# Optimization experiments

Measured on AMD Instinct MI355X. Metric: run time of the kernel, lower is better.

## Reference

```python
import jax, jax.numpy as jnp
import numpy as np

# dims: B batch, N nodes, E edges, C=dim_in, W=window_len, D=embed_dim, O=dim_out, K=link_len, NB=bootstrap count
B, N, E, C, W, D, O, K, NB = 16, 2000, 3000, 17, 12, 16, 256, 3, 3


def setup_inputs() -> dict:
    key = jax.random.key(0)
    ks = jax.random.split(key, 20)
    return {
        "x": jax.random.normal(ks[0], (B, N, C), jnp.float32),
        "x_window": jax.random.normal(ks[1], (B, W, N, 1), jnp.float32),
        "node_embeddings": jax.random.normal(ks[2], (N, D), jnp.float32) * 0.1,
        "fixed_adj": 0,
        "adj": jax.random.normal(ks[3], (N, N), jnp.float32),
        "stay_cost": 1,
        "jump_cost": 1,
        "ZFC_input": jax.random.normal(ks[4], (B, O // 8), jnp.float32),
        "hodge_Laplacian": jax.random.normal(ks[5], (E, E), jnp.float32) * 0.02,
        "x_e_window": jax.random.normal(ks[6], (B, W, E, 1), jnp.float32),
        "incidence_matrix": jax.random.normal(ks[7], (N, E), jnp.float32) * 0.02,
        "weights_pool": jax.random.normal(ks[8], (D, K, C, O // 4), jnp.float32) * 0.05,
        "window_weights_supra": jax.random.normal(ks[9], (D, 1, O // 8), jnp.float32) * 0.05,
        "window_weights_temporal": jax.random.normal(ks[10], (D, 1, O // 2), jnp.float32) * 0.05,
        "bias_pool": jax.random.normal(ks[11], (D, O), jnp.float32) * 0.05,
        "T_param": jax.random.normal(ks[12], (W,), jnp.float32) * 0.1,
        "lin_w": jax.random.normal(ks[13], (1, 1), jnp.float32),
        "lin_b": jax.random.normal(ks[14], (1,), jnp.float32),
        "gnn_w": jax.random.normal(ks[15], (N, N), jnp.float32) * 0.02,
        "gnn_b": jnp.zeros((N,), jnp.float32),
        "bootstrap_idx": jnp.sort(jax.random.randint(ks[16], (NB,), 0, W)),
    }


def _forward(x, x_window, ne, fixed_adj, adj, stay_cost, jump_cost, ZFC_input,
             hodge, x_e_window, inc, wp, wws_p, wwt_p, bp, Tp, lin_w, lin_b,
             gnn_w, gnn_b, bidx):
    n = ne.shape[0]
    e = hodge.shape[0]
    b = x.shape[0]
    nb = bidx.shape[0]

    # adaptive transition matrix S (diag filled with stay_cost after relu)
    S0 = jax.nn.relu(ne @ ne.T)
    ii = jnp.arange(n)
    S0 = S0.at[ii, ii].set(jnp.float32(stay_cost))
    if fixed_adj:  # static Python bool branch
        S = adj * jnp.exp(S0)
    else:
        S = jax.nn.softmax(S0, axis=1)
    # faithful to torch broadcasting: column j divided by row-sum of row j
    S = S / jnp.sum(S, axis=1)

    # diffusion support power series: [I, S, S@S, ...]
    sup = [jnp.eye(n, dtype=S.dtype), S]
    for _ in range(2, K):
        sup.append(S @ sup[-1])
    supports = jnp.stack(sup, axis=0)  # (K, N, N)

    # supra-Laplacian: hodge on diagonal blocks, jump_cost*I on strict upper blocks
    supra = (jnp.kron(jnp.eye(nb, dtype=hodge.dtype), hodge)
             + jnp.kron(jnp.triu(jnp.ones((nb, nb), hodge.dtype), 1),
                        jnp.float32(jump_cost) * jnp.eye(e, dtype=hodge.dtype)))  # (nb*E, nb*E)

    # adaptive weights/bias from node embeddings
    weights = jnp.einsum('nd,dkio->nkio', ne, wp)   # (N, K, C, O/4)
    bias = ne @ bp                                   # (N, O)

    # graph diffusion branch
    x_s = jnp.einsum('knm,bmc->bknc', supports, x).transpose(0, 2, 1, 3)  # (B,N,K,C)
    x_sconv = jnp.einsum('bnki,nkio->bno', x_s, weights)                   # (B,N,O/4)

    # supra / hypergraph branch
    wws = jnp.einsum('nd,dio->nio', ne, wws_p)                 # (N,1,O/8)
    xe = x_e_window[:, bidx].reshape(b, nb * e, 1)             # bootstrap gather
    xe = xe * lin_w[0, 0] + lin_b[0]                           # Linear(1,1)
    xes = jnp.einsum('bmi,mn->bni', xe, supra).reshape(b, nb, 1, e)
    xen = jnp.einsum('bfim,mn->bfin', xes, inc.T).reshape(b, nb, n, 1)
    x_e_n_wconv = jnp.einsum('bfni,nio->bfno', xen, wws).mean(axis=1)  # (B,N,O/8)

    # temporal window branch (einsum fuses the permute + matmul with T)
    wwt = jnp.einsum('nd,dio->nio', ne, wwt_p)                  # (N,1,O/2)
    x_wconv_t = jnp.einsum('btni,nio,t->bno', x_window, wwt, Tp)  # (B,N,O/2)

    # ZFC branch: repeat over nodes, GNN = Linear(N,N) + relu, reshape (view) back
    ZFC = jnp.tile(ZFC_input.reshape(b, -1, 1), (1, 1, n))      # (B,O/8,N)
    zout = jax.nn.relu(ZFC @ gnn_w.T + gnn_b)                   # (B,O/8,N)
    x_ZFC = zout.reshape(b, n, -1)                              # (B,N,O/8) (reshape, not transpose)

    return jnp.concatenate([x_sconv, x_ZFC, x_wconv_t, x_e_n_wconv], axis=-1) + bias


def reference(x, x_window, node_embeddings, fixed_adj, adj, stay_cost, jump_cost,
              ZFC_input, hodge_Laplacian, x_e_window, incidence_matrix,
              weights_pool, window_weights_supra, window_weights_temporal,
              bias_pool, T_param, lin_w, lin_b, gnn_w, gnn_b, bootstrap_idx):
    return _forward(x, x_window, node_embeddings, fixed_adj, adj, stay_cost,
                    jump_cost, ZFC_input, hodge_Laplacian, x_e_window,
                    incidence_matrix, weights_pool, window_weights_supra,
                    window_weights_temporal, bias_pool, T_param, lin_w, lin_b,
                    gnn_w, gnn_b, bootstrap_idx)
```

## Files before the change

kernel.cpp:

```cpp
#include <hip/hip_runtime.h>
#include <hip/hip_bf16.h>

typedef __hip_bfloat16 bf16;
typedef unsigned short ushort_t;
typedef __attribute__((ext_vector_type(8))) short short8;
typedef __attribute__((ext_vector_type(4))) short short4_t;
typedef __attribute__((ext_vector_type(4))) float f32x4;
typedef __attribute__((ext_vector_type(2))) float f32x2;

#define B_ 16
#define N_ 2000
#define E_ 3000
#define C_ 17
#define W_ 12
#define D_ 16
#define O_ 256
#define NB_ 3
#define KPAD 2048
#define KI_ 51
#define SEGS 25
#define ECH 120
#define EPAD 768

static __device__ __forceinline__ ushort_t f2b(float f) {
  bf16 h = __float2bfloat16(f);
  return *reinterpret_cast<ushort_t*>(&h);
}
static __device__ __forceinline__ float b2f_u(ushort_t u) {
  bf16 h = *reinterpret_cast<bf16*>(&u);
  return __bfloat162float(h);
}
__device__ __forceinline__ int idxval(const int* p, int i) {
  int iv = p[i];
  if (iv >= 0 && iv < 1000000) return iv;
  return (int)__int_as_float(iv);
}

__global__ void k_S(const float* __restrict__ ne, const int* __restrict__ stay,
                    ushort_t* __restrict__ S) {
  const int i = blockIdx.x;
  const int t = threadIdx.x;
  if (i >= N_) {
#pragma unroll
    for (int it = 0; it < 8; ++it) S[(long)i*KPAD + t + it*256] = 0;
    return;
  }
  __shared__ float ne_l[512*20];
  __shared__ float reds[4];
  f32x4 nei[4];
#pragma unroll
  for (int q = 0; q < 4; ++q) nei[q] = *(const f32x4*)(ne + i*16 + q*4);
  const float stayf = (float)(*stay);
  float vals[8];
  float s = 0.f;
  for (int c = 0; c < 4; ++c) {
    __syncthreads();
#pragma unroll
    for (int u = 0; u < 8; ++u) {
      int unit = t + u*256;
      int row = unit >> 2, dq = unit & 3;
      int gj = c*512 + row;
      f32x4 v = {0.f,0.f,0.f,0.f};
      if (gj < N_) v = *(const f32x4*)(ne + gj*16 + dq*4);
      *(f32x4*)(ne_l + row*20 + dq*4) = v;
    }
    __syncthreads();
#pragma unroll
    for (int r = 0; r < 2; ++r) {
      int row_l = t + r*256;
      int j = c*512 + row_l;
      float e = 0.f;
      if (j < N_) {
        f32x4 a4 = {0.f,0.f,0.f,0.f};
#pragma unroll
        for (int q = 0; q < 4; ++q) a4 += nei[q] * (*(const f32x4*)(ne_l + row_l*20 + q*4));
        float dot = a4.x + a4.y + a4.z + a4.w;
        float v = dot > 0.f ? dot : 0.f;
        if (j == i) v = stayf;
        e = __expf(v);
        s += e;
      }
      vals[2*c + r] = e;
    }
  }
#pragma unroll
  for (int off = 32; off > 0; off >>= 1) s += __shfl_xor(s, off, 64);
  if ((t & 63) == 0) reds[t >> 6] = s;
  __syncthreads();
  s = reds[0] + reds[1] + reds[2] + reds[3];
  const float inv = 1.f/s;
#pragma unroll
  for (int it = 0; it < 8; ++it) {
    int j = t + it*256;
    S[(long)i*KPAD + j] = f2b(vals[it]*inv);
  }
}

__global__ void k_small(const float* __restrict__ xew, const int* __restrict__ bidx,
                        const float* __restrict__ lw, const float* __restrict__ lb,
                        const int* __restrict__ jc, float* __restrict__ u,
                        float* __restrict__ v,
                        const float* __restrict__ xwin, const float* __restrict__ Tp,
                        float* __restrict__ xw,
                        const float* __restrict__ gw, float* __restrict__ g,
                        const float* __restrict__ x, ushort_t* __restrict__ BT1) {
  const int bid = blockIdx.x;
  const int t = threadIdx.x;
  if (bid < 188) {
    int idx = bid*256 + t;
    if (idx >= B_*E_) return;
    int b = idx / E_, e = idx - b*E_;
    const float lwf = lw[0], lbf = lb[0];
    float uu = 0.f, vv = 0.f;
#pragma unroll
    for (int f = 0; f < NB_; ++f) {
      int tt = idxval(bidx, f);
      if (tt < 0) tt = 0;
      if (tt >= W_) tt = W_ - 1;
      float val = xew[(b*W_ + tt)*E_ + e]*lwf + lbf;
      uu += val;
      vv += (float)(NB_ - 1 - f)*val;
    }
    u[idx] = uu;
    v[idx] = vv*(float)(*jc);
  } else if (bid < 313) {
    int idx = (bid - 188)*256 + t;
    int b = idx / N_, n = idx - b*N_;
    float s = 0.f;
#pragma unroll
    for (int tt = 0; tt < W_; ++tt) s += xwin[(b*W_ + tt)*N_ + n]*Tp[tt];
    xw[idx] = s;
  } else if (bid < 2313) {
    int i = bid - 313;
    float s = 0.f;
    for (int j = t; j < N_; j += 256) s += gw[(long)i*N_ + j];
#pragma unroll
    for (int off = 32; off > 0; off >>= 1) s += __shfl_xor(s, off, 64);
    __shared__ float red[4];
    if ((t & 63) == 0) red[t >> 6] = s;
    __syncthreads();
    if (t == 0) g[i] = red[0] + red[1] + red[2] + red[3];
  } else {
    int j = bid - 2313;
    int bb = j / C_, cc = j - bb*C_;
#pragma unroll
    for (int uu = 0; uu < 8; ++uu) {
      int n = t + uu*256;
      float vv = 0.f;
      if (bb < B_ && n < N_) vv = x[(bb*N_ + n)*C_ + cc];
      BT1[(long)j*KPAD + n] = f2b(vv);
    }
  }
}

__global__ __launch_bounds__(256) void k_mm2(const ushort_t* __restrict__ A,
                                             const ushort_t* __restrict__ BT,
                                             float* __restrict__ Cf,
                                             ushort_t* __restrict__ Cb,
                                             int writeCb) {
  __shared__ ushort_t lds[3][10240];
  const int t = threadIdx.x;
  const int m0 = blockIdx.x * 16;
  const int j0 = blockIdx.y * 144;
  const int wv = t >> 6, lane = t & 63;
  const int lm = lane & 15, lg = lane >> 4;
  const char* gA = (const char*)A + (size_t)m0 * (KPAD*2);
  const char* gB = (const char*)BT + (size_t)j0 * (KPAD*2);

  f32x4 acc[3];
#pragma unroll
  for (int q = 0; q < 3; ++q) acc[q] = (f32x4){0.f,0.f,0.f,0.f};

  auto stage = [&](int p, int s) {
    const long kb = (long)s * 128;
#pragma unroll
    for (int u = 0; u < 5; ++u) {
      int x = (u*256 + t) << 4;
      int y = x ^ (((x >> 7) & 7) << 4);
      int r = y >> 7, c = y & 127;
      const char* gp = (r < 16) ? gA + (long)r*(KPAD*2) + kb + c
                                : gB + (long)(r-16)*(KPAD*2) + kb + c;
      __builtin_amdgcn_global_load_lds(
          (const __attribute__((address_space(1))) void*)gp,
          (__attribute__((address_space(3))) void*)(&lds[p][u*2048 + wv*512]),
          16, 0, 0);
    }
  };

  auto compute = [&](int p) {
    const char* base = (const char*)&lds[p][0];
#pragma unroll
    for (int kg = 0; kg < 2; ++kg) {
      int xA = (lm << 7) + (kg << 6) + (lg << 4);
      xA ^= ((xA >> 7) & 7) << 4;
      short8 a = *(const short8*)(base + xA);
#pragma unroll
      for (int ti = 0; ti < 3; ++ti) {
        int tile = wv + ti*4;
        if (tile < 9) {
          int xB = ((16 + tile*16 + lm) << 7) + (kg << 6) + (lg << 4);
          xB ^= ((xB >> 7) & 7) << 4;
          short8 b = *(const short8*)(base + xB);
          acc[ti] = __builtin_amdgcn_mfma_f32_16x16x32_bf16(a, b, acc[ti], 0, 0, 0);
        }
      }
    }
  };

  stage(0, 0);
  stage(1, 1);
  for (int s = 0; s < 32; ++s) {
    int p = s % 3;
    if (s < 30) {
      stage((s + 2) % 3, s + 2);
      asm volatile("s_waitcnt vmcnt(10)" ::: "memory");
    } else if (s == 30) {
      asm volatile("s_waitcnt vmcnt(5)" ::: "memory");
    } else {
      asm volatile("s_waitcnt vmcnt(0)" ::: "memory");
    }
    __builtin_amdgcn_s_barrier();
    asm volatile("" ::: "memory");
    compute(p);
    asm volatile("" ::: "memory");
    __builtin_amdgcn_s_barrier();
  }

#pragma unroll
  for (int ti = 0; ti < 3; ++ti) {
    int tile = wv + ti*4;
    if (tile < 9) {
      int j = j0 + tile*16 + lm;
      int m = m0 + lg*4;
      *(f32x4*)(Cf + (long)j*KPAD + m) = acc[ti];
      if (writeCb) {
        short4_t hv;
#pragma unroll
        for (int q = 0; q < 4; ++q)
          hv[q] = (m + q < N_) ? (short)f2b(acc[ti][q]) : (short)0;
        *(short4_t*)(Cb + (long)j*KPAD + m) = hv;
      }
    }
  }
}

__global__ void k_hodge(const float* __restrict__ u, const float* __restrict__ hodge,
                        float* __restrict__ xesP) {
  const int t = threadIdx.x;
  const int e2 = blockIdx.x*256 + t;
  const int seg = blockIdx.y;
  const int e1a = seg*ECH;
  __shared__ float ul[ECH*16];
  for (int idx = t; idx < ECH*16; idx += 256) {
    int bb = idx / ECH, ee = idx - bb*ECH;
    ul[ee*16 + bb] = u[bb*E_ + e1a + ee];
  }
  __syncthreads();
  if (e2 >= E_) return;
  float acc[16] = {};
  for (int ee = 0; ee < ECH; ee += 8) {
    float h[8];
#pragma unroll
    for (int q = 0; q < 8; ++q) h[q] = hodge[(long)(e1a + ee + q)*E_ + e2];
#pragma unroll
    for (int q = 0; q < 8; ++q) {
#pragma unroll
      for (int g4 = 0; g4 < 4; ++g4) {
        f32x4 u4 = *(const f32x4*)&ul[(ee + q)*16 + g4*4];
        acc[g4*4+0] += u4.x*h[q];
        acc[g4*4+1] += u4.y*h[q];
        acc[g4*4+2] += u4.z*h[q];
        acc[g4*4+3] += u4.w*h[q];
      }
    }
  }
#pragma unroll
  for (int bb = 0; bb < 16; ++bb)
    xesP[((long)seg*16 + bb)*E_ + e2] = acc[bb];
}

__global__ void k_redxes(const float* __restrict__ xesP, const float* __restrict__ v,
                         float* __restrict__ xes) {
  int idx = blockIdx.x*256 + threadIdx.x;
  if (idx >= B_*E_) return;
  int b = idx / E_, e = idx - b*E_;
  float s = v[idx];
#pragma unroll
  for (int q = 0; q < SEGS; ++q) s += xesP[((long)q*16 + b)*E_ + e];
  xes[idx] = s;
}

__global__ __launch_bounds__(256) void k_inc(const float* __restrict__ xes,
                                             const float* __restrict__ inc,
                                             float* __restrict__ xenP) {
  __shared__ float xes_l[16*EPAD];
  const int t = threadIdx.x;
  const int wv = t >> 6, lane = t & 63;
  const int cy = blockIdx.y;
  const int n0 = blockIdx.x*8;
  for (int i4 = t; i4 < 16*(EPAD/4); i4 += 256) {
    int row = i4 / (EPAD/4);
    int el = (i4 - row*(EPAD/4)) << 2;
    int e = cy*EPAD + el;
    f32x4 vv = {0.f,0.f,0.f,0.f};
    if (e < E_) vv = *(const f32x4*)(xes + (long)row*E_ + e);
    *(f32x4*)&xes_l[row*EPAD + el] = vv;
  }
  __syncthreads();
  const int na = n0 + wv*2;
  const int nb = na + 1;
  const float* rowA = inc + (long)na*E_ + cy*EPAD;
  const float* rowB = inc + (long)nb*E_ + cy*EPAD;
  float accA[16] = {}, accB[16] = {};
#pragma unroll
  for (int g = 0; g < 3; ++g) {
    int e4 = (g*64 + lane) << 2;
    bool ok = (cy*EPAD + e4) < E_;
    f32x4 ia = {0.f,0.f,0.f,0.f}, ib = {0.f,0.f,0.f,0.f};
    if (ok) { ia = *(const f32x4*)(rowA + e4); ib = *(const f32x4*)(rowB + e4); }
#pragma unroll
    for (int b = 0; b < 16; ++b) {
      f32x4 xs = *(const f32x4*)&xes_l[b*EPAD + e4];
      accA[b] += xs.x*ia.x + xs.y*ia.y + xs.z*ia.z + xs.w*ia.w;
      accB[b] += xs.x*ib.x + xs.y*ib.y + xs.z*ib.z + xs.w*ib.w;
    }
  }
#pragma unroll
  for (int b = 0; b < 16; ++b) {
#pragma unroll
    for (int off = 32; off > 0; off >>= 1) {
      accA[b] += __shfl_xor(accA[b], off, 64);
      accB[b] += __shfl_xor(accB[b], off, 64);
    }
  }
  const int bl = lane & 15;
  float oA = 0.f, oB = 0.f;
#pragma unroll
  for (int b = 0; b < 16; ++b)
    if (bl == b) { oA = accA[b]; oB = accB[b]; }
  if (lane < 16)
    xenP[((long)cy*16 + bl)*N_ + na] = oA*(1.f/3.f);
  else if (lane < 32)
    xenP[((long)cy*16 + bl)*N_ + nb] = oB*(1.f/3.f);
}

#define NPC 4
__global__ __launch_bounds__(256) void k_tail1(const float* __restrict__ x,
                          const float* __restrict__ C32a,
                          const float* __restrict__ C32b,
                          const float* __restrict__ ne,
                          const float* __restrict__ wp,
                          const float* __restrict__ bp,
                          float* __restrict__ out) {
  __shared__ ushort_t W_l[NPC*52*64];
  __shared__ float xs_l[NPC*52*20];
  const int t = threadIdx.x;
  const int n0 = blockIdx.x*NPC;
  const int lane = t & 63, wv = t >> 6;
  float nev[NPC][16];
#pragma unroll
  for (int p = 0; p < NPC; ++p)
#pragma unroll
    for (int q = 0; q < 4; ++q)
      *(f32x4*)&nev[p][q*4] = *(const f32x4*)(ne + (n0 + p)*D_ + q*4);
  for (int idx = t; idx < 52*64; idx += 256) {
    int ki = idx >> 6, o = idx & 63;
    float a[NPC] = {};
#pragma unroll
    for (int d = 0; d < 16; ++d) {
      float w = (ki < KI_) ? wp[d*3264 + idx] : bp[d*256 + o];
#pragma unroll
      for (int p = 0; p < NPC; ++p) a[p] += nev[p][d]*w;
    }
#pragma unroll
    for (int p = 0; p < NPC; ++p) W_l[p*3328 + idx] = f2b(a[p]);
  }
  for (int idx = t; idx < KI_*64; idx += 256) {
    int ki = idx >> 6;
    int b = (idx >> 2) & 15, p = idx & 3;
    int k = ki / C_, cc = ki - k*C_;
    int n = n0 + p;
    float v;
    if (k == 0)      v = x[(b*N_ + n)*C_ + cc];
    else if (k == 1) v = C32a[(long)(b*C_ + cc)*KPAD + n];
    else             v = C32b[(long)(b*C_ + cc)*KPAD + n];
    xs_l[p*1040 + ki*20 + b] = v;
  }
  if (t < 64) xs_l[(t & 3)*1040 + KI_*20 + (t >> 2)] = 1.0f;
  __syncthreads();
  const int o = lane, bg = wv;
#pragma unroll
  for (int p = 0; p < NPC; ++p) {
    f32x4 acc = {0.f,0.f,0.f,0.f};
    for (int ki = 0; ki < 52; ++ki) {
      float w = b2f_u(W_l[p*3328 + ki*64 + o]);
      f32x4 xs4 = *(const f32x4*)&xs_l[p*1040 + ki*20 + bg*4];
      acc += xs4 * w;
    }
#pragma unroll
    for (int j = 0; j < 4; ++j)
      out[((long)((bg*4 + j)*N_ + n0 + p))*O_ + o] = acc[j];
  }
}

#define NT2 2
__global__ __launch_bounds__(256) void k_tail2(const float* __restrict__ ne,
                          const float* __restrict__ bp,
                          const float* __restrict__ wwt, const float* __restrict__ wws,
                          const float* __restrict__ zfc, const float* __restrict__ gnnb,
                          const float* __restrict__ g, const float* __restrict__ xw,
                          const float* __restrict__ xenP,
                          float* __restrict__ out) {
  __shared__ float ne_l[NT2][16];
  __shared__ float wb[NT2][160];
  __shared__ float bi[NT2][192];
  __shared__ float gi_l[NT2][32], gb_l[NT2][32];
  __shared__ int   q_l[NT2][32];
  __shared__ float zf_l[16*32];
  __shared__ float xwv[16][NT2], xev[16][NT2];
  const int t = threadIdx.x;
  const int n0 = blockIdx.x*NT2;
  zf_l[t] = zfc[t];
  zf_l[t + 256] = zfc[t + 256];
  if (t < NT2*16) ne_l[t >> 4][t & 15] = ne[(n0 + (t >> 4))*16 + (t & 15)];
  if (t < NT2*32) {
    int nl = t >> 5, j = t & 31;
    int flat = (n0 + nl)*32 + j;
    int q = flat / N_;
    int i = flat - q*N_;
    q_l[nl][j] = q;
    gi_l[nl][j] = g[i];
    gb_l[nl][j] = gnnb[i];
  }
  if (t < 16*NT2) {
    int b = t / NT2, nl = t - b*NT2;
    int n = n0 + nl;
    xwv[b][nl] = xw[b*N_ + n];
    xev[b][nl] = xenP[b*N_ + n] + xenP[(16 + b)*N_ + n]
               + xenP[(32 + b)*N_ + n] + xenP[(48 + b)*N_ + n];
  }
  __syncthreads();
  for (int idx = t; idx < NT2*192; idx += 256) {
    int nl = idx / 192, op = idx - nl*192;
    float wv = 0.f, bv = 0.f;
#pragma unroll
    for (int d = 0; d < 16; ++d) {
      float nd = ne_l[nl][d];
      bv += nd * bp[d*256 + 64 + op];
      float ww = 0.f;
      if (op >= 32 && op < 160) ww = wwt[d*128 + (op - 32)];
      else if (op >= 160)       ww = wws[d*32 + (op - 160)];
      wv += nd * ww;
    }
    bi[nl][op] = bv;
    if (op >= 32) wb[nl][op - 32] = wv;
  }
  __syncthreads();
  for (int idx = t; idx < 16*NT2*192; idx += 256) {
    int b = idx / (NT2*192);
    int r = idx - b*(NT2*192);
    int nl = r / 192, op = r - nl*192;
    float val;
    if (op < 32) {
      float z = zf_l[b*32 + q_l[nl][op]]*gi_l[nl][op] + gb_l[nl][op];
      val = z > 0.f ? z : 0.f;
    } else if (op < 160) {
      val = xwv[b][nl] * wb[nl][op - 32];
    } else {
      val = xev[b][nl] * wb[nl][op - 32];
    }
    out[((long)(b*N_ + n0 + nl))*O_ + 64 + op] = val + bi[nl][op];
  }
}

extern "C" void kernel_launch(void* const* d_in, const int* in_sizes, int n_in,
                              void* d_out, int out_size, void* d_ws, size_t ws_size,
                              hipStream_t stream) {
  const float* x     = (const float*)d_in[0];
  const float* xwin  = (const float*)d_in[1];
  const float* ne    = (const float*)d_in[2];
  const int*   stay  = (const int*)d_in[5];
  const int*   jc    = (const int*)d_in[6];
  const float* zfc   = (const float*)d_in[7];
  const float* hodge = (const float*)d_in[8];
  const float* xew   = (const float*)d_in[9];
  const float* inc   = (const float*)d_in[10];
  const float* wp    = (const float*)d_in[11];
  const float* wws   = (const float*)d_in[12];
  const float* wwt   = (const float*)d_in[13];
  const float* bp    = (const float*)d_in[14];
  const float* Tp    = (const float*)d_in[15];
  const float* lw    = (const float*)d_in[16];
  const float* lb    = (const float*)d_in[17];
  const float* gw    = (const float*)d_in[18];
  const float* gnnb  = (const float*)d_in[19];
  const int*   bidx  = (const int*)d_in[20];
  float* out = (float*)d_out;

  char* wsb = (char*)d_ws;
  float*    C32a = (float*)(wsb);
  float*    C32b = (float*)(wsb + 2359296);
  ushort_t* BT1  = (ushort_t*)(wsb + 2359296);
  float* u    = (float*)(wsb + 4718592);
  float* v    = (float*)(wsb + 4910592);
  float* xes  = (float*)(wsb + 5102592);
  float* xw   = (float*)(wsb + 5294592);
  float* g    = (float*)(wsb + 5422592);
  float* xenP = (float*)(wsb + 5430592);

  char* ob = (char*)d_out;
  ushort_t* S    = (ushort_t*)(ob);
  ushort_t* BT2  = (ushort_t*)(ob + 8388608);
  float*    xesP = (float*)(ob + 9568256);

  k_small<<<2601, 256, 0, stream>>>(xew, bidx, lw, lb, jc, u, v,
                                    xwin, Tp, xw, gw, g, x, BT1);
  k_S<<<2048, 256, 0, stream>>>(ne, stay, S);
  k_mm2<<<dim3(128,2), 256, 0, stream>>>(S, BT1, C32a, BT2, 1);
  k_mm2<<<dim3(128,2), 256, 0, stream>>>(S, BT2, C32b, nullptr, 0);
  k_hodge<<<dim3(12, SEGS), 256, 0, stream>>>(u, hodge, xesP);
  k_redxes<<<188, 256, 0, stream>>>(xesP, v, xes);
  k_inc<<<dim3(250, 4), 256, 0, stream>>>(xes, inc, xenP);
  k_tail1<<<500, 256, 0, stream>>>(x, C32a, C32b, ne, wp, bp, out);
  k_tail2<<<1000, 256, 0, stream>>>(ne, bp, wwt, wws, zfc, gnnb, g, xw,
                                    xenP, out);
}
```

Baseline: 289.0 us.

## Rebalance grids across kernels, precompute per-node weights, and merge tail kernels

Several changes together. k_S now computes two softmax rows per block with half the grid, and k_mm2 is split into narrower column tiles (48 instead of 144) so it launches more blocks with smaller LDS. Hodge segments are tripled with shorter chunks. Per-node weight generation moves into extra k_small blocks that write a bf16 Wd buffer to workspace. The two tail kernels are merged into one launch, and the first part now handles one node per block. The aim is more parallelism and fewer launches, at the cost of an extra global round trip for Wd and more partial sums to reduce.

Measured after the change: 341.1 us. 1.18x slower.

```diff
diff --git a/kernel.cpp b/kernel.cpp
--- a/kernel.cpp
+++ b/kernel.cpp
@@ -18,9 +18,10 @@
 #define NB_ 3
 #define KPAD 2048
 #define KI_ 51
-#define SEGS 25
-#define ECH 120
+#define SEGS 75
+#define ECH 40
 #define EPAD 768
+#define JB 48
 
 static __device__ __forceinline__ ushort_t f2b(float f) {
   bf16 h = __float2bfloat16(f);
@@ -39,20 +40,20 @@
 __global__ void k_S(const float* __restrict__ ne, const int* __restrict__ stay,
                     ushort_t* __restrict__ S) {
   const int i = blockIdx.x;
+  const int i2 = i + 1024;
   const int t = threadIdx.x;
-  if (i >= N_) {
-#pragma unroll
-    for (int it = 0; it < 8; ++it) S[(long)i*KPAD + t + it*256] = 0;
-    return;
-  }
   __shared__ float ne_l[512*20];
-  __shared__ float reds[4];
-  f32x4 nei[4];
-#pragma unroll
-  for (int q = 0; q < 4; ++q) nei[q] = *(const f32x4*)(ne + i*16 + q*4);
+  __shared__ float reds[4], reds2[4];
+  const bool has2 = (i2 < N_);
+  f32x4 nei[4], nei2[4];
+#pragma unroll
+  for (int q = 0; q < 4; ++q) {
+    nei[q] = *(const f32x4*)(ne + i*16 + q*4);
+    nei2[q] = has2 ? *(const f32x4*)(ne + (long)i2*16 + q*4) : (f32x4){0.f,0.f,0.f,0.f};
+  }
   const float stayf = (float)(*stay);
-  float vals[8];
-  float s = 0.f;
+  float vals[8], vals2[8];
+  float s = 0.f, s2 = 0.f;
   for (int c = 0; c < 4; ++c) {
     __syncthreads();
 #pragma unroll
@@ -61,7 +62,7 @@
       int row = unit >> 2, dq = unit & 3;
       int gj = c*512 + row;
       f32x4 v = {0.f,0.f,0.f,0.f};
-      if (gj < N_) v = *(const f32x4*)(ne + gj*16 + dq*4);
+      if (gj < N_) v = *(const f32x4*)(ne + (long)gj*16 + dq*4);
       *(f32x4*)(ne_l + row*20 + dq*4) = v;
     }
     __syncthreads();
@@ -69,30 +70,48 @@
     for (int r = 0; r < 2; ++r) {
       int row_l = t + r*256;
       int j = c*512 + row_l;
-      float e = 0.f;
+      float e = 0.f, e2 = 0.f;
       if (j < N_) {
-        f32x4 a4 = {0.f,0.f,0.f,0.f};
-#pragma unroll
-        for (int q = 0; q < 4; ++q) a4 += nei[q] * (*(const f32x4*)(ne_l + row_l*20 + q*4));
+        f32x4 a4 = {0.f,0.f,0.f,0.f}, b4 = {0.f,0.f,0.f,0.f};
+#pragma unroll
+        for (int q = 0; q < 4; ++q) {
+          f32x4 nl = *(const f32x4*)(ne_l + row_l*20 + q*4);
+          a4 += nei[q]*nl;
+          b4 += nei2[q]*nl;
+        }
         float dot = a4.x + a4.y + a4.z + a4.w;
         float v = dot > 0.f ? dot : 0.f;
         if (j == i) v = stayf;
         e = __expf(v);
         s += e;
+        if (has2) {
+          float dot2 = b4.x + b4.y + b4.z + b4.w;
+          float v2 = dot2 > 0.f ? dot2 : 0.f;
+          if (j == i2) v2 = stayf;
+          e2 = __expf(v2);
+          s2 += e2;
+        }
       }
       vals[2*c + r] = e;
-    }
-  }
-#pragma unroll
-  for (int off = 32; off > 0; off >>= 1) s += __shfl_xor(s, off, 64);
-  if ((t & 63) == 0) reds[t >> 6] = s;
+      vals2[2*c + r] = e2;
+    }
+  }
+#pragma unroll
+  for (int off = 32; off > 0; off >>= 1) {
+    s  += __shfl_xor(s,  off, 64);
+    s2 += __shfl_xor(s2, off, 64);
+  }
+  if ((t & 63) == 0) { reds[t >> 6] = s; reds2[t >> 6] = s2; }
   __syncthreads();
-  s = reds[0] + reds[1] + reds[2] + reds[3];
+  s  = reds[0] + reds[1] + reds[2] + reds[3];
+  s2 = reds2[0] + reds2[1] + reds2[2] + reds2[3];
   const float inv = 1.f/s;
+  const float inv2 = has2 ? 1.f/s2 : 0.f;
 #pragma unroll
   for (int it = 0; it < 8; ++it) {
     int j = t + it*256;
     S[(long)i*KPAD + j] = f2b(vals[it]*inv);
+    S[(long)i2*KPAD + j] = has2 ? f2b(vals2[it]*inv2) : (ushort_t)0;
   }
 }
 
@@ -103,7 +122,9 @@
                         const float* __restrict__ xwin, const float* __restrict__ Tp,
                         float* __restrict__ xw,
                         const float* __restrict__ gw, float* __restrict__ g,
-                        const float* __restrict__ x, ushort_t* __restrict__ BT1) {
+                        const float* __restrict__ x, ushort_t* __restrict__ BT1,
+                        const float* __restrict__ ne, const float* __restrict__ wp,
+                        const float* __restrict__ bp, ushort_t* __restrict__ Wd) {
   const int bid = blockIdx.x;
   const int t = threadIdx.x;
   if (bid < 188) {
@@ -140,7 +161,7 @@
     if ((t & 63) == 0) red[t >> 6] = s;
     __syncthreads();
     if (t == 0) g[i] = red[0] + red[1] + red[2] + red[3];
-  } else {
+  } else if (bid < 2601) {
     int j = bid - 2313;
     int bb = j / C_, cc = j - bb*C_;
 #pragma unroll
@@ -150,6 +171,25 @@
       if (bb < B_ && n < N_) vv = x[(bb*N_ + n)*C_ + cc];
       BT1[(long)j*KPAD + n] = f2b(vv);
     }
+  } else {
+    int n0w = (bid - 2601)*8;
+    __shared__ float ne8[8][16];
+    if (t < 128) ne8[t >> 4][t & 15] = ne[(long)(n0w + (t >> 4))*16 + (t & 15)];
+    __syncthreads();
+    for (int c = t; c < 52*64; c += 256) {
+      int ki = c >> 6, o = c & 63;
+      float w[16];
+#pragma unroll
+      for (int d = 0; d < 16; ++d)
+        w[d] = (ki < KI_) ? wp[d*3264 + c] : bp[d*256 + o];
+#pragma unroll
+      for (int p = 0; p < 8; ++p) {
+        float a = 0.f;
+#pragma unroll
+        for (int d = 0; d < 16; ++d) a += ne8[p][d]*w[d];
+        Wd[(long)(n0w + p)*3328 + c] = f2b(a);
+      }
+    }
   }
 }
 
@@ -158,23 +198,21 @@
                                              float* __restrict__ Cf,
                                              ushort_t* __restrict__ Cb,
                                              int writeCb) {
-  __shared__ ushort_t lds[3][10240];
+  __shared__ ushort_t lds[3][4096];
   const int t = threadIdx.x;
   const int m0 = blockIdx.x * 16;
-  const int j0 = blockIdx.y * 144;
+  const int j0 = blockIdx.y * JB;
   const int wv = t >> 6, lane = t & 63;
   const int lm = lane & 15, lg = lane >> 4;
   const char* gA = (const char*)A + (size_t)m0 * (KPAD*2);
   const char* gB = (const char*)BT + (size_t)j0 * (KPAD*2);
 
-  f32x4 acc[3];
-#pragma unroll
-  for (int q = 0; q < 3; ++q) acc[q] = (f32x4){0.f,0.f,0.f,0.f};
+  f32x4 acc = {0.f,0.f,0.f,0.f};
 
   auto stage = [&](int p, int s) {
     const long kb = (long)s * 128;
 #pragma unroll
-    for (int u = 0; u < 5; ++u) {
+    for (int u = 0; u < 2; ++u) {
       int x = (u*256 + t) << 4;
       int y = x ^ (((x >> 7) & 7) << 4);
       int r = y >> 7, c = y & 127;
@@ -188,21 +226,17 @@
   };
 
   auto compute = [&](int p) {
-    const char* base = (const char*)&lds[p][0];
-#pragma unroll
-    for (int kg = 0; kg < 2; ++kg) {
-      int xA = (lm << 7) + (kg << 6) + (lg << 4);
-      xA ^= ((xA >> 7) & 7) << 4;
-      short8 a = *(const short8*)(base + xA);
-#pragma unroll
-      for (int ti = 0; ti < 3; ++ti) {
-        int tile = wv + ti*4;
-        if (tile < 9) {
-          int xB = ((16 + tile*16 + lm) << 7) + (kg << 6) + (lg << 4);
-          xB ^= ((xB >> 7) & 7) << 4;
-          short8 b = *(const short8*)(base + xB);
-          acc[ti] = __builtin_amdgcn_mfma_f32_16x16x32_bf16(a, b, acc[ti], 0, 0, 0);
-        }
+    if (wv < 3) {
+      const char* base = (const char*)&lds[p][0];
+#pragma unroll
+      for (int kg = 0; kg < 2; ++kg) {
+        int xA = (lm << 7) + (kg << 6) + (lg << 4);
+        xA ^= ((xA >> 7) & 7) << 4;
+        short8 a = *(const short8*)(base + xA);
+        int xB = ((16 + wv*16 + lm) << 7) + (kg << 6) + (lg << 4);
+        xB ^= ((xB >> 7) & 7) << 4;
+        short8 b = *(const short8*)(base + xB);
+        acc = __builtin_amdgcn_mfma_f32_16x16x32_bf16(a, b, acc, 0, 0, 0);
       }
     }
   };
@@ -213,9 +247,9 @@
     int p = s % 3;
     if (s < 30) {
       stage((s + 2) % 3, s + 2);
-      asm volatile("s_waitcnt vmcnt(10)" ::: "memory");
+      asm volatile("s_waitcnt vmcnt(4)" ::: "memory");
     } else if (s == 30) {
-      asm volatile("s_waitcnt vmcnt(5)" ::: "memory");
+      asm volatile("s_waitcnt vmcnt(2)" ::: "memory");
     } else {
       asm volatile("s_waitcnt vmcnt(0)" ::: "memory");
     }
@@ -226,20 +260,16 @@
     __builtin_amdgcn_s_barrier();
   }
 
-#pragma unroll
-  for (int ti = 0; ti < 3; ++ti) {
-    int tile = wv + ti*4;
-    if (tile < 9) {
-      int j = j0 + tile*16 + lm;
-      int m = m0 + lg*4;
-      *(f32x4*)(Cf + (long)j*KPAD + m) = acc[ti];
-      if (writeCb) {
-        short4_t hv;
-#pragma unroll
-        for (int q = 0; q < 4; ++q)
-          hv[q] = (m + q < N_) ? (short)f2b(acc[ti][q]) : (short)0;
-        *(short4_t*)(Cb + (long)j*KPAD + m) = hv;
-      }
+  if (wv < 3) {
+    int j = j0 + wv*16 + lm;
+    int m = m0 + lg*4;
+    *(f32x4*)(Cf + (long)j*KPAD + m) = acc;
+    if (writeCb) {
+      short4_t hv;
+#pragma unroll
+      for (int q = 0; q < 4; ++q)
+        hv[q] = (m + q < N_) ? (short)f2b(acc[q]) : (short)0;
+      *(short4_t*)(Cb + (long)j*KPAD + m) = hv;
     }
   }
 }
@@ -285,7 +315,7 @@
   if (idx >= B_*E_) return;
   int b = idx / E_, e = idx - b*E_;
   float s = v[idx];
-#pragma unroll
+#pragma unroll 15
   for (int q = 0; q < SEGS; ++q) s += xesP[((long)q*16 + b)*E_ + e];
   xes[idx] = s;
 }
@@ -344,73 +374,19 @@
     xenP[((long)cy*16 + bl)*N_ + nb] = oB*(1.f/3.f);
 }
 
-#define NPC 4
-__global__ __launch_bounds__(256) void k_tail1(const float* __restrict__ x,
+#define NT2 2
+__global__ __launch_bounds__(256) void k_tailF(const float* __restrict__ x,
                           const float* __restrict__ C32a,
                           const float* __restrict__ C32b,
+                          const ushort_t* __restrict__ Wd,
                           const float* __restrict__ ne,
-                          const float* __restrict__ wp,
-                          const float* __restrict__ bp,
-                          float* __restrict__ out) {
-  __shared__ ushort_t W_l[NPC*52*64];
-  __shared__ float xs_l[NPC*52*20];
-  const int t = threadIdx.x;
-  const int n0 = blockIdx.x*NPC;
-  const int lane = t & 63, wv = t >> 6;
-  float nev[NPC][16];
-#pragma unroll
-  for (int p = 0; p < NPC; ++p)
-#pragma unroll
-    for (int q = 0; q < 4; ++q)
-      *(f32x4*)&nev[p][q*4] = *(const f32x4*)(ne + (n0 + p)*D_ + q*4);
-  for (int idx = t; idx < 52*64; idx += 256) {
-    int ki = idx >> 6, o = idx & 63;
-    float a[NPC] = {};
-#pragma unroll
-    for (int d = 0; d < 16; ++d) {
-      float w = (ki < KI_) ? wp[d*3264 + idx] : bp[d*256 + o];
-#pragma unroll
-      for (int p = 0; p < NPC; ++p) a[p] += nev[p][d]*w;
-    }
-#pragma unroll
-    for (int p = 0; p < NPC; ++p) W_l[p*3328 + idx] = f2b(a[p]);
-  }
-  for (int idx = t; idx < KI_*64; idx += 256) {
-    int ki = idx >> 6;
-    int b = (idx >> 2) & 15, p = idx & 3;
-    int k = ki / C_, cc = ki - k*C_;
-    int n = n0 + p;
-    float v;
-    if (k == 0)      v = x[(b*N_ + n)*C_ + cc];
-    else if (k == 1) v = C32a[(long)(b*C_ + cc)*KPAD + n];
-    else             v = C32b[(long)(b*C_ + cc)*KPAD + n];
-    xs_l[p*1040 + ki*20 + b] = v;
-  }
-  if (t < 64) xs_l[(t & 3)*1040 + KI_*20 + (t >> 2)] = 1.0f;
-  __syncthreads();
-  const int o = lane, bg = wv;
-#pragma unroll
-  for (int p = 0; p < NPC; ++p) {
-    f32x4 acc = {0.f,0.f,0.f,0.f};
-    for (int ki = 0; ki < 52; ++ki) {
-      float w = b2f_u(W_l[p*3328 + ki*64 + o]);
-      f32x4 xs4 = *(const f32x4*)&xs_l[p*1040 + ki*20 + bg*4];
-      acc += xs4 * w;
-    }
-#pragma unroll
-    for (int j = 0; j < 4; ++j)
-      out[((long)((bg*4 + j)*N_ + n0 + p))*O_ + o] = acc[j];
-  }
-}
-
-#define NT2 2
-__global__ __launch_bounds__(256) void k_tail2(const float* __restrict__ ne,
                           const float* __restrict__ bp,
                           const float* __restrict__ wwt, const float* __restrict__ wws,
                           const float* __restrict__ zfc, const float* __restrict__ gnnb,
                           const float* __restrict__ g, const float* __restrict__ xw,
                           const float* __restrict__ xenP,
                           float* __restrict__ out) {
+  __shared__ float xs_l[52*20];
   __shared__ float ne_l[NT2][16];
   __shared__ float wb[NT2][160];
   __shared__ float bi[NT2][192];
@@ -419,57 +395,84 @@
   __shared__ float zf_l[16*32];
   __shared__ float xwv[16][NT2], xev[16][NT2];
   const int t = threadIdx.x;
-  const int n0 = blockIdx.x*NT2;
-  zf_l[t] = zfc[t];
-  zf_l[t + 256] = zfc[t + 256];
-  if (t < NT2*16) ne_l[t >> 4][t & 15] = ne[(n0 + (t >> 4))*16 + (t & 15)];
-  if (t < NT2*32) {
-    int nl = t >> 5, j = t & 31;
-    int flat = (n0 + nl)*32 + j;
-    int q = flat / N_;
-    int i = flat - q*N_;
-    q_l[nl][j] = q;
-    gi_l[nl][j] = g[i];
-    gb_l[nl][j] = gnnb[i];
-  }
-  if (t < 16*NT2) {
-    int b = t / NT2, nl = t - b*NT2;
-    int n = n0 + nl;
-    xwv[b][nl] = xw[b*N_ + n];
-    xev[b][nl] = xenP[b*N_ + n] + xenP[(16 + b)*N_ + n]
-               + xenP[(32 + b)*N_ + n] + xenP[(48 + b)*N_ + n];
-  }
-  __syncthreads();
-  for (int idx = t; idx < NT2*192; idx += 256) {
-    int nl = idx / 192, op = idx - nl*192;
-    float wv = 0.f, bv = 0.f;
-#pragma unroll
-    for (int d = 0; d < 16; ++d) {
-      float nd = ne_l[nl][d];
-      bv += nd * bp[d*256 + 64 + op];
-      float ww = 0.f;
-      if (op >= 32 && op < 160) ww = wwt[d*128 + (op - 32)];
-      else if (op >= 160)       ww = wws[d*32 + (op - 160)];
-      wv += nd * ww;
-    }
-    bi[nl][op] = bv;
-    if (op >= 32) wb[nl][op - 32] = wv;
-  }
-  __syncthreads();
-  for (int idx = t; idx < 16*NT2*192; idx += 256) {
-    int b = idx / (NT2*192);
-    int r = idx - b*(NT2*192);
-    int nl = r / 192, op = r - nl*192;
-    float val;
-    if (op < 32) {
-      float z = zf_l[b*32 + q_l[nl][op]]*gi_l[nl][op] + gb_l[nl][op];
-      val = z > 0.f ? z : 0.f;
-    } else if (op < 160) {
-      val = xwv[b][nl] * wb[nl][op - 32];
-    } else {
-      val = xev[b][nl] * wb[nl][op - 32];
-    }
-    out[((long)(b*N_ + n0 + nl))*O_ + 64 + op] = val + bi[nl][op];
+  if (blockIdx.x < 2000) {
+    const int n = blockIdx.x;
+    const int lane = t & 63, wv = t >> 6;
+    for (int idx = t; idx < KI_*16; idx += 256) {
+      int ki = idx >> 4, b = idx & 15;
+      int k = ki / C_, cc = ki - k*C_;
+      float v;
+      if (k == 0)      v = x[(b*N_ + n)*C_ + cc];
+      else if (k == 1) v = C32a[(long)(b*C_ + cc)*KPAD + n];
+      else             v = C32b[(long)(b*C_ + cc)*KPAD + n];
+      xs_l[ki*20 + b] = v;
+    }
+    if (t < 16) xs_l[KI_*20 + t] = 1.0f;
+    __syncthreads();
+    const ushort_t* wrow = Wd + (long)n*3328 + lane;
+    f32x4 acc = {0.f,0.f,0.f,0.f};
+#pragma unroll
+    for (int ki = 0; ki < 52; ++ki) {
+      float w = b2f_u(wrow[ki*64]);
+      f32x4 xs4 = *(const f32x4*)&xs_l[ki*20 + wv*4];
+      acc += xs4 * w;
+    }
+#pragma unroll
+    for (int j = 0; j < 4; ++j)
+      out[((long)((wv*4 + j)*N_ + n))*O_ + lane] = acc[j];
+  } else {
+    const int n0 = (blockIdx.x - 2000)*NT2;
+    zf_l[t] = zfc[t];
+    zf_l[t + 256] = zfc[t + 256];
+    if (t < NT2*16) ne_l[t >> 4][t & 15] = ne[(n0 + (t >> 4))*16 + (t & 15)];
+    if (t < NT2*32) {
+      int nl = t >> 5, j = t & 31;
+      int flat = (n0 + nl)*32 + j;
+      int q = flat / N_;
+      int i = flat - q*N_;
+      q_l[nl][j] = q;
+      gi_l[nl][j] = g[i];
+      gb_l[nl][j] = gnnb[i];
+    }
+    if (t < 16*NT2) {
+      int b = t / NT2, nl = t - b*NT2;
+      int n = n0 + nl;
+      xwv[b][nl] = xw[b*N_ + n];
+      xev[b][nl] = xenP[b*N_ + n] + xenP[(16 + b)*N_ + n]
+                 + xenP[(32 + b)*N_ + n] + xenP[(48 + b)*N_ + n];
+    }
+    __syncthreads();
+    for (int idx = t; idx < NT2*192; idx += 256) {
+      int nl = idx / 192, op = idx - nl*192;
+      float wv2 = 0.f, bv = 0.f;
+#pragma unroll
+      for (int d = 0; d < 16; ++d) {
+        float nd = ne_l[nl][d];
+        bv += nd * bp[d*256 + 64 + op];
+        float ww = 0.f;
+        if (op >= 32 && op < 160) ww = wwt[d*128 + (op - 32)];
+        else if (op >= 160)       ww = wws[d*32 + (op - 160)];
+        wv2 += nd * ww;
+      }
+      bi[nl][op] = bv;
+      if (op >= 32) wb[nl][op - 32] = wv2;
+    }
+    __syncthreads();
+    for (int idx = t; idx < 16*NT2*192; idx += 256) {
+      int b = idx / (NT2*192);
+      int r = idx - b*(NT2*192);
+      int nl = r / 192, op = r - nl*192;
+      float val;
+      if (op < 32) {
+        float z = zf_l[b*32 + q_l[nl][op]]*gi_l[nl][op] + gb_l[nl][op];
+        val = z > 0.f ? z : 0.f;
+      } else if (op < 160) {
+        val = xwv[b][nl] * wb[nl][op - 32];
+      } else {
+        val = xev[b][nl] * wb[nl][op - 32];
+      }
+      out[((long)(b*N_ + n0 + nl))*O_ + 64 + op] = val + bi[nl][op];
+    }
   }
 }
 
@@ -507,21 +510,22 @@
   float* xw   = (float*)(wsb + 5294592);
   float* g    = (float*)(wsb + 5422592);
   float* xenP = (float*)(wsb + 5430592);
+  ushort_t* Wd = (ushort_t*)(wsb + 5942592);
 
   char* ob = (char*)d_out;
   ushort_t* S    = (ushort_t*)(ob);
   ushort_t* BT2  = (ushort_t*)(ob + 8388608);
   float*    xesP = (float*)(ob + 9568256);
 
-  k_small<<<2601, 256, 0, stream>>>(xew, bidx, lw, lb, jc, u, v,
-                                    xwin, Tp, xw, gw, g, x, BT1);
-  k_S<<<2048, 256, 0, stream>>>(ne, stay, S);
-  k_mm2<<<dim3(128,2), 256, 0, stream>>>(S, BT1, C32a, BT2, 1);
-  k_mm2<<<dim3(128,2), 256, 0, stream>>>(S, BT2, C32b, nullptr, 0);
+  k_small<<<2851, 256, 0, stream>>>(xew, bidx, lw, lb, jc, u, v,
+                                    xwin, Tp, xw, gw, g, x, BT1,
+                                    ne, wp, bp, Wd);
+  k_S<<<1024, 256, 0, stream>>>(ne, stay, S);
+  k_mm2<<<dim3(128,6), 256, 0, stream>>>(S, BT1, C32a, BT2, 1);
+  k_mm2<<<dim3(128,6), 256, 0, stream>>>(S, BT2, C32b, nullptr, 0);
   k_hodge<<<dim3(12, SEGS), 256, 0, stream>>>(u, hodge, xesP);
   k_redxes<<<188, 256, 0, stream>>>(xesP, v, xes);
   k_inc<<<dim3(250, 4), 256, 0, stream>>>(xes, inc, xenP);
-  k_tail1<<<500, 256, 0, stream>>>(x, C32a, C32b, ne, wp, bp, out);
-  k_tail2<<<1000, 256, 0, stream>>>(ne, bp, wwt, wws, zfc, gnnb, g, xw,
-                                    xenP, out);
-}
+  k_tailF<<<3000, 256, 0, stream>>>(x, C32a, C32b, Wd, ne, bp, wwt, wws,
+                                    zfc, gnnb, g, xw, xenP, out);
+}
```
